# Performance work log

Measured on AMD Instinct MI355X. Metric: run time of the kernel, lower is better.

Reference implementation:

```python
import jax, jax.numpy as jnp
import numpy as np

B, T, D = 2, 2048, 1024
H = 16
HD = D // H  # 128
L = 8  # latent prefix length
SCALE = HD ** -0.5


def setup_inputs() -> dict:
    key = jax.random.key(0)
    ks = jax.random.split(key, 12)
    p = lambda k, shape: jax.random.normal(k, shape, dtype=jnp.float32) * 0.02
    return {
        "hidden_states": jax.random.normal(ks[0], (B, T, D), dtype=jnp.float32),
        "decoder_latent": jax.random.normal(ks[1], (B, H, L, 2 * HD), dtype=jnp.float32),
        "attention_mask": jnp.zeros((B, 1, T, L + T), dtype=jnp.float32),
        "Wq": p(ks[2], (D, D)), "bq": p(ks[3], (D,)),
        "Wk": p(ks[4], (D, D)), "bk": p(ks[5], (D,)),
        "Wv": p(ks[6], (D, D)), "bv": p(ks[7], (D,)),
        "Wo": p(ks[8], (D, D)), "bo": p(ks[9], (D,)),
    }


def _heads(x):
    # [B, S, D] -> [B, H, S, HD]
    return x.reshape(x.shape[0], x.shape[1], H, HD).transpose(0, 2, 1, 3)


def reference(hidden_states, decoder_latent, attention_mask,
              Wq, bq, Wk, bk, Wv, bv, Wo, bo):
    q = _heads((hidden_states @ Wq + bq) * SCALE)            # [B,H,T,HD]
    k = _heads(hidden_states @ Wk + bk)                      # [B,H,T,HD]
    v = _heads(hidden_states @ Wv + bv)
    lk, lv = jnp.split(decoder_latent, 2, axis=-1)           # [B,H,L,HD] each
    k = jnp.concatenate([lk, k], axis=2)                     # [B,H,L+T,HD]
    v = jnp.concatenate([lv, v], axis=2)
    scores = jnp.einsum('bhtd,bhsd->bhts', q, k) + attention_mask
    probs = jax.nn.softmax(scores, axis=-1)                  # [B,H,T,L+T]
    o = jnp.einsum('bhts,bhsd->bhtd', probs, v)              # [B,H,T,HD]
    o = o.transpose(0, 2, 1, 3).reshape(hidden_states.shape[0], -1, D)
    return o @ Wo + bo
```

## Files before the change

### kernel.cpp

```cpp
#include <hip/hip_runtime.h>

#define T_ 2048
#define D_ 1024
#define H_ 16
#define HD_ 64
#define L_ 8
#define S_ 2056
#define M_ 4096
#define SCALE_ 0.125f

typedef unsigned short u16;
typedef u16 u16x4 __attribute__((ext_vector_type(4)));
typedef u16 u16x8 __attribute__((ext_vector_type(8)));
typedef __bf16 bf16x8 __attribute__((ext_vector_type(8)));
typedef float f32x4 __attribute__((ext_vector_type(4)));

#define MFMA(a, b, c) __builtin_amdgcn_mfma_f32_16x16x32_bf16((a), (b), (c), 0, 0, 0)

__device__ __forceinline__ u16 f2bf(float x) {
    unsigned u = __float_as_uint(x);
    return (u16)((u + 0x7fffu + ((u >> 16) & 1u)) >> 16);
}
__device__ __forceinline__ bf16x8 ldfrag(const u16* p) {
    u16x8 u = *(const u16x8*)p;
    return __builtin_bit_cast(bf16x8, u);
}

__global__ __launch_bounds__(256) void cvt_hidden(const float* __restrict__ hs,
                                                  u16* __restrict__ Hh) {
    size_t i4 = (size_t)blockIdx.x * 256 + threadIdx.x;
    f32x4 v = ((const f32x4*)hs)[i4];
    u16x4 hi;
#pragma unroll
    for (int j = 0; j < 4; ++j) hi[j] = f2bf(v[j]);
    ((u16x4*)Hh)[i4] = hi;
}

__global__ __launch_bounds__(256) void tr_w(const float* __restrict__ Wq, const float* __restrict__ Wk,
                                            const float* __restrict__ Wv, const float* __restrict__ Wo,
                                            u16* __restrict__ WT) {
    const int z = blockIdx.z;
    const float* W = (z == 0) ? Wq : (z == 1) ? Wk : (z == 2) ? Wv : Wo;
    u16* WTh = WT + (size_t)z * 1048576u;
    __shared__ float t_s[64][68];
    const int k0 = blockIdx.y * 64, n0 = blockIdx.x * 64;
    const int tid = threadIdx.x;
#pragma unroll
    for (int p = 0; p < 4; ++p) {
        int slot = tid + p * 256;
        int kr = slot >> 4, seg = slot & 15;
        *(f32x4*)&t_s[kr][seg * 4] = *(const f32x4*)(W + (size_t)(k0 + kr) * D_ + n0 + seg * 4);
    }
    __syncthreads();
#pragma unroll
    for (int p = 0; p < 4; ++p) {
        int slot = tid + p * 256;
        int nr = slot >> 4, ks = slot & 15;
        u16x4 hi;
#pragma unroll
        for (int j = 0; j < 4; ++j) hi[j] = f2bf(t_s[ks * 4 + j][nr]);
        *(u16x4*)(WTh + (size_t)(n0 + nr) * D_ + k0 + ks * 4) = hi;
    }
}

__device__ __forceinline__ void gemm_core_1t(const u16* __restrict__ Ah, const u16* __restrict__ BTh,
                                             int bm, int bn, f32x4 acc[4][4]) {
    __shared__ u16 As1[128][40];
    __shared__ u16 Bs1[128][40];
    const int tid = threadIdx.x;
    const int lane = tid & 63, w = tid >> 6;
    const int wm = w >> 1, wn = w & 1;
    const int c = lane & 15, rg = lane >> 4;
    for (int k0 = 0; k0 < D_; k0 += 32) {
        __syncthreads();
#pragma unroll
        for (int i = 0; i < 2; ++i) {
            int slot = tid + i * 256;
            int r = slot >> 2, q = slot & 3;
            *(u16x8*)&As1[r][q * 8] = *(const u16x8*)(Ah + (size_t)(bm * 128 + r) * D_ + k0 + q * 8);
            *(u16x8*)&Bs1[r][q * 8] = *(const u16x8*)(BTh + (size_t)(bn * 128 + r) * D_ + k0 + q * 8);
        }
        __syncthreads();
        bf16x8 af[4], bf[4];
#pragma unroll
        for (int mi = 0; mi < 4; ++mi) af[mi] = ldfrag(&As1[wm * 64 + mi * 16 + c][8 * rg]);
#pragma unroll
        for (int ni = 0; ni < 4; ++ni) bf[ni] = ldfrag(&Bs1[wn * 64 + ni * 16 + c][8 * rg]);
#pragma unroll
        for (int mi = 0; mi < 4; ++mi) {
#pragma unroll
            for (int ni = 0; ni < 4; ++ni) acc[mi][ni] = MFMA(af[mi], bf[ni], acc[mi][ni]);
        }
    }
}

__global__ __launch_bounds__(256) void gemm_qkv(
    const u16* __restrict__ Ah, const u16* __restrict__ WT,
    const float* __restrict__ bq, const float* __restrict__ bk, const float* __restrict__ bv,
    u16* __restrict__ Qh, u16* __restrict__ Kh, u16* __restrict__ Vh) {
    const int z = blockIdx.z;
    const u16* BTh = WT + (size_t)z * 1048576u;
    f32x4 acc[4][4];
    f32x4 zero = {0.f, 0.f, 0.f, 0.f};
#pragma unroll
    for (int a = 0; a < 4; ++a)
#pragma unroll
        for (int b2 = 0; b2 < 4; ++b2) acc[a][b2] = zero;
    gemm_core_1t(Ah, BTh, blockIdx.y, blockIdx.x, acc);
    const int lane = threadIdx.x & 63, w = threadIdx.x >> 6;
    const int wm = w >> 1, wn = w & 1, c = lane & 15, rg = lane >> 4;
    const float* bias = (z == 0) ? bq : ((z == 1) ? bk : bv);
#pragma unroll
    for (int ni = 0; ni < 4; ++ni) {
        int n = blockIdx.x * 128 + wn * 64 + ni * 16 + c;
        float bb = bias[n];
        int hh = n >> 6, hd = n & 63;
#pragma unroll
        for (int mi = 0; mi < 4; ++mi) {
#pragma unroll
            for (int r = 0; r < 4; ++r) {
                int m = blockIdx.y * 128 + wm * 64 + mi * 16 + rg * 4 + r;
                int batch = m >> 11, t = m & 2047;
                float val = acc[mi][ni][r] + bb;
                if (z == 0) {
                    Qh[((size_t)(batch * H_ + hh) * T_ + t) * HD_ + hd] = f2bf(val * SCALE_);
                } else {
                    size_t o = ((size_t)(batch * H_ + hh) * S_ + (t + L_)) * HD_ + hd;
                    if (z == 1) Kh[o] = f2bf(val);
                    else        Vh[o] = f2bf(val);
                }
            }
        }
    }
}

__global__ __launch_bounds__(256) void latent_fill(const float* __restrict__ lat,
                                                   u16* __restrict__ Kh, u16* __restrict__ Vh) {
    int i = blockIdx.x * 256 + threadIdx.x;
    float v = lat[i];
    int cc = i & 127, l = (i >> 7) & 7, h = (i >> 10) & 15, b = i >> 14;
    size_t o = ((size_t)(b * H_ + h) * S_ + l) * HD_ + (cc & 63);
    if (cc < 64) Kh[o] = f2bf(v);
    else         Vh[o] = f2bf(v);
}

__global__ __launch_bounds__(256) void tr_v(const u16* __restrict__ Vh, u16* __restrict__ VTh) {
    const int bh = blockIdx.y;
    const int s0 = blockIdx.x * 64;
    const int tid = threadIdx.x;
    __shared__ u16 t_s[64][72];
#pragma unroll
    for (int p = 0; p < 2; ++p) {
        int slot = tid + p * 256;
        int sr = slot >> 3, seg = slot & 7;
        int s = s0 + sr;
        u16x8 v = {0, 0, 0, 0, 0, 0, 0, 0};
        if (s < S_) v = *(const u16x8*)(Vh + ((size_t)bh * S_ + s) * HD_ + seg * 8);
        *(u16x8*)&t_s[sr][seg * 8] = v;
    }
    __syncthreads();
#pragma unroll
    for (int p = 0; p < 2; ++p) {
        int slot = tid + p * 256;
        int hd = slot & 63, sc = slot >> 6;
        if (s0 + sc * 8 < S_) {
            u16x8 v;
#pragma unroll
            for (int j = 0; j < 8; ++j) v[j] = t_s[sc * 8 + j][hd];
            *(u16x8*)(VTh + ((size_t)bh * HD_ + hd) * S_ + s0 + sc * 8) = v;
        }
    }
}

__global__ __launch_bounds__(256) void attn(
    const u16* __restrict__ Qh, const u16* __restrict__ Kh,
    const u16* __restrict__ VTh, const float* __restrict__ mask, u16* __restrict__ Oh) {
    __shared__ u16 Ks[64][64];
    __shared__ u16 Vs[64][64];
    __shared__ u16 Ps[4][16][64];
    const int tid = threadIdx.x, lane = tid & 63, w = tid >> 6;
    const int bh = blockIdx.y, b = bh >> 4, h = bh & 15;
    const int t0 = blockIdx.x * 64;
    const int c = lane & 15, rg = lane >> 4;
    const int c7 = c & 7;

    bf16x8 qh[2];
    {
        const int t = t0 + w * 16 + c;
        const size_t qbase = ((size_t)bh * T_ + t) * HD_;
        qh[0] = ldfrag(Qh + qbase + 8 * rg);
        qh[1] = ldfrag(Qh + qbase + 32 + 8 * rg);
    }
    f32x4 oa[4];
    f32x4 zero = {0.f, 0.f, 0.f, 0.f};
#pragma unroll
    for (int f = 0; f < 4; ++f) oa[f] = zero;
    float lrun[4] = {0.f, 0.f, 0.f, 0.f};
    const float* mrow[4];
#pragma unroll
    for (int r = 0; r < 4; ++r)
        mrow[r] = mask + ((size_t)b * T_ + t0 + w * 16 + rg * 4 + r) * S_;

    for (int s0 = 0; s0 < S_; s0 += 64) {
        __syncthreads();
#pragma unroll
        for (int i = 0; i < 2; ++i) {
            int slot = tid + i * 256;
            int row = (slot >> 3) & 63, seg = slot & 7;
            int s = s0 + row;
            u16x8 v = {0, 0, 0, 0, 0, 0, 0, 0};
            if (s < S_) v = *(const u16x8*)(Kh + ((size_t)bh * S_ + s) * HD_ + seg * 8);
            *(u16x8*)&Ks[row][(seg ^ (row & 7)) * 8] = v;
        }
#pragma unroll
        for (int i = 0; i < 2; ++i) {
            int slot = tid + i * 256;
            int row = (slot >> 3) & 63, seg = slot & 7;
            int ss = s0 + seg * 8;
            u16x8 v = {0, 0, 0, 0, 0, 0, 0, 0};
            if (ss < S_) v = *(const u16x8*)(VTh + ((size_t)bh * HD_ + row) * S_ + ss);
            *(u16x8*)&Vs[row][(seg ^ (row & 7)) * 8] = v;
        }
        float mreg[4][4];
#pragma unroll
        for (int r = 0; r < 4; ++r) {
#pragma unroll
            for (int cf = 0; cf < 4; ++cf) {
                int sa = s0 + cf * 16 + c;
                mreg[r][cf] = (sa < S_) ? (mrow[r][sa] - 8.0f) : -1e30f;
            }
        }
        __syncthreads();

        f32x4 sc[4];
#pragma unroll
        for (int cf = 0; cf < 4; ++cf) sc[cf] = zero;
#pragma unroll
        for (int ks = 0; ks < 2; ++ks) {
#pragma unroll
            for (int cf = 0; cf < 4; ++cf) {
                int g = ((ks * 4 + rg) ^ c7) * 8;
                bf16x8 kf = ldfrag(&Ks[cf * 16 + c][g]);
                sc[cf] = MFMA(qh[ks], kf, sc[cf]);
            }
        }
#pragma unroll
        for (int r = 0; r < 4; ++r) {
#pragma unroll
            for (int cf = 0; cf < 4; ++cf) sc[cf][r] = __expf(sc[cf][r] + mreg[r][cf]);
            lrun[r] += (sc[0][r] + sc[1][r]) + (sc[2][r] + sc[3][r]);
        }
#pragma unroll
        for (int r = 0; r < 4; ++r) {
            int prow = rg * 4 + r;
#pragma unroll
            for (int cf = 0; cf < 4; ++cf) {
                int pg = (cf * 2 + (c >> 3)) ^ (prow & 7);
                Ps[w][prow][pg * 8 + c7] = (u16)(__float_as_uint(sc[cf][r]) >> 16);
            }
        }
#pragma unroll
        for (int kf = 0; kf < 2; ++kf) {
            int g = ((kf * 4 + rg) ^ c7) * 8;
            bf16x8 pa = ldfrag(&Ps[w][c][g]);
#pragma unroll
            for (int f = 0; f < 4; ++f) {
                bf16x8 vh = ldfrag(&Vs[f * 16 + c][g]);
                oa[f] = MFMA(pa, vh, oa[f]);
            }
        }
    }
#pragma unroll
    for (int mm = 1; mm < 16; mm <<= 1) {
#pragma unroll
        for (int r = 0; r < 4; ++r) lrun[r] += __shfl_xor(lrun[r], mm);
    }
#pragma unroll
    for (int r = 0; r < 4; ++r) lrun[r] = 1.0f / lrun[r];
#pragma unroll
    for (int f = 0; f < 4; ++f) {
#pragma unroll
        for (int r = 0; r < 4; ++r) {
            int tg = t0 + w * 16 + rg * 4 + r;
            int col = h * HD_ + f * 16 + c;
            Oh[((size_t)b * T_ + tg) * D_ + col] = f2bf(oa[f][r] * lrun[r]);
        }
    }
}

__global__ __launch_bounds__(256) void gemm_fin(
    const u16* __restrict__ Ah, const u16* __restrict__ BTh,
    const float* __restrict__ bo, float* __restrict__ out) {
    f32x4 acc[4][4];
    f32x4 zero = {0.f, 0.f, 0.f, 0.f};
#pragma unroll
    for (int a = 0; a < 4; ++a)
#pragma unroll
        for (int b2 = 0; b2 < 4; ++b2) acc[a][b2] = zero;
    gemm_core_1t(Ah, BTh, blockIdx.y, blockIdx.x, acc);
    const int lane = threadIdx.x & 63, w = threadIdx.x >> 6;
    const int wm = w >> 1, wn = w & 1, c = lane & 15, rg = lane >> 4;
#pragma unroll
    for (int ni = 0; ni < 4; ++ni) {
        int n = blockIdx.x * 128 + wn * 64 + ni * 16 + c;
        float bb = bo[n];
#pragma unroll
        for (int mi = 0; mi < 4; ++mi) {
#pragma unroll
            for (int r = 0; r < 4; ++r) {
                int m = blockIdx.y * 128 + wm * 64 + mi * 16 + rg * 4 + r;
                out[(size_t)m * D_ + n] = acc[mi][ni][r] + bb;
            }
        }
    }
}

extern "C" void kernel_launch(void* const* d_in, const int* in_sizes, int n_in,
                              void* d_out, int out_size, void* d_ws, size_t ws_size,
                              hipStream_t stream) {
    (void)in_sizes; (void)n_in; (void)out_size;
    if (ws_size < 50429952ull) return;
    const float* hs  = (const float*)d_in[0];
    const float* lat = (const float*)d_in[1];
    const float* msk = (const float*)d_in[2];
    const float* Wq = (const float*)d_in[3];
    const float* bq = (const float*)d_in[4];
    const float* Wk = (const float*)d_in[5];
    const float* bk = (const float*)d_in[6];
    const float* Wv = (const float*)d_in[7];
    const float* bv = (const float*)d_in[8];
    const float* Wo = (const float*)d_in[9];
    const float* bo = (const float*)d_in[10];
    float* out = (float*)d_out;
    char* ws = (char*)d_ws;

    u16* Hh  = (u16*)(ws + 0ull);
    u16* WT  = (u16*)(ws + 8388608ull);
    u16* Qh  = (u16*)(ws + 16777216ull);
    u16* Kh  = (u16*)(ws + 25165824ull);
    u16* Vh  = (u16*)(ws + 33587200ull);
    u16* VTh = (u16*)(ws + 42008576ull);
    u16* Oh  = Hh;

    cvt_hidden<<<4096, 256, 0, stream>>>(hs, Hh);
    tr_w<<<dim3(16, 16, 4), 256, 0, stream>>>(Wq, Wk, Wv, Wo, WT);
    gemm_qkv<<<dim3(8, 32, 3), 256, 0, stream>>>(Hh, WT, bq, bk, bv, Qh, Kh, Vh);
    latent_fill<<<128, 256, 0, stream>>>(lat, Kh, Vh);
    tr_v<<<dim3(33, 32), 256, 0, stream>>>(Vh, VTh);
    attn<<<dim3(32, 32), 256, 0, stream>>>(Qh, Kh, VTh, msk, Oh);
    gemm_fin<<<dim3(8, 32), 256, 0, stream>>>(Oh, WT + 3u * 1048576u, bo, out);
}
```

Measured before the change: 408.2 us.

## Double-buffer attention K/V tiles with direct global-to-LDS loads

The attention kernel now keeps two LDS buffers for K and V and issues the next tile's loads with global_load_lds (direct to LDS) before computing on the current tile. This drops to one barrier per iteration and lets memory latency overlap with the MFMA and softmax work. Out-of-range rows are clamped to valid addresses instead of zero-filled, which relies on the mask and zero probabilities to cancel them. LDS use doubles for K/V, which may lower occupancy. Correctness also depends on the load-count waits being placed before the barrier.

Result: slower. 464.8 us (+13.9%).

```diff
diff --git a/kernel.cpp b/kernel.cpp
--- a/kernel.cpp
+++ b/kernel.cpp
@@ -24,6 +24,11 @@
 __device__ __forceinline__ bf16x8 ldfrag(const u16* p) {
     u16x8 u = *(const u16x8*)p;
     return __builtin_bit_cast(bf16x8, u);
+}
+__device__ __forceinline__ void g2lds16(const u16* g, u16* l) {
+    __builtin_amdgcn_global_load_lds(
+        (const __attribute__((address_space(1))) void*)g,
+        (__attribute__((address_space(3))) void*)l, 16, 0, 0);
 }
 
 __global__ __launch_bounds__(256) void cvt_hidden(const float* __restrict__ hs,
@@ -175,8 +180,8 @@
 __global__ __launch_bounds__(256) void attn(
     const u16* __restrict__ Qh, const u16* __restrict__ Kh,
     const u16* __restrict__ VTh, const float* __restrict__ mask, u16* __restrict__ Oh) {
-    __shared__ u16 Ks[64][64];
-    __shared__ u16 Vs[64][64];
+    __shared__ u16 Ks[2][64][64];
+    __shared__ u16 Vs[2][64][64];
     __shared__ u16 Ps[4][16][64];
     const int tid = threadIdx.x, lane = tid & 63, w = tid >> 6;
     const int bh = blockIdx.y, b = bh >> 4, h = bh & 15;
@@ -184,6 +189,23 @@
     const int c = lane & 15, rg = lane >> 4;
     const int c7 = c & 7;
 
+    const int srow_o = lane >> 3;
+    const int sseg   = lane & 7;
+
+    auto STAGE = [&](int bufi, int s0n) {
+#pragma unroll
+        for (int i = 0; i < 2; ++i) {
+            int row = w * 16 + i * 8 + srow_o;
+            int sg = sseg ^ (row & 7);
+            int sK = s0n + row;
+            sK = (sK < S_) ? sK : (S_ - 1);
+            g2lds16(Kh + ((size_t)bh * S_ + sK) * HD_ + sg * 8, &Ks[bufi][w * 16 + i * 8][0]);
+            int sV = s0n + sg * 8;
+            sV = (sV <= S_ - 8) ? sV : (S_ - 8);
+            g2lds16(VTh + ((size_t)bh * HD_ + row) * S_ + sV, &Vs[bufi][w * 16 + i * 8][0]);
+        }
+    };
+
     bf16x8 qh[2];
     {
         const int t = t0 + w * 16 + c;
@@ -201,26 +223,14 @@
     for (int r = 0; r < 4; ++r)
         mrow[r] = mask + ((size_t)b * T_ + t0 + w * 16 + rg * 4 + r) * S_;
 
-    for (int s0 = 0; s0 < S_; s0 += 64) {
-        __syncthreads();
-#pragma unroll
-        for (int i = 0; i < 2; ++i) {
-            int slot = tid + i * 256;
-            int row = (slot >> 3) & 63, seg = slot & 7;
-            int s = s0 + row;
-            u16x8 v = {0, 0, 0, 0, 0, 0, 0, 0};
-            if (s < S_) v = *(const u16x8*)(Kh + ((size_t)bh * S_ + s) * HD_ + seg * 8);
-            *(u16x8*)&Ks[row][(seg ^ (row & 7)) * 8] = v;
-        }
-#pragma unroll
-        for (int i = 0; i < 2; ++i) {
-            int slot = tid + i * 256;
-            int row = (slot >> 3) & 63, seg = slot & 7;
-            int ss = s0 + seg * 8;
-            u16x8 v = {0, 0, 0, 0, 0, 0, 0, 0};
-            if (ss < S_) v = *(const u16x8*)(VTh + ((size_t)bh * HD_ + row) * S_ + ss);
-            *(u16x8*)&Vs[row][(seg ^ (row & 7)) * 8] = v;
-        }
+    STAGE(0, 0);
+    __syncthreads();
+    int buf = 0;
+
+    for (int t = 0; t < 33; ++t) {
+        const int s0 = t * 64;
+        if (t + 1 < 33) STAGE(buf ^ 1, s0 + 64);
+
         float mreg[4][4];
 #pragma unroll
         for (int r = 0; r < 4; ++r) {
@@ -230,7 +240,6 @@
                 mreg[r][cf] = (sa < S_) ? (mrow[r][sa] - 8.0f) : -1e30f;
             }
         }
-        __syncthreads();
 
         f32x4 sc[4];
 #pragma unroll
@@ -240,7 +249,7 @@
 #pragma unroll
             for (int cf = 0; cf < 4; ++cf) {
                 int g = ((ks * 4 + rg) ^ c7) * 8;
-                bf16x8 kf = ldfrag(&Ks[cf * 16 + c][g]);
+                bf16x8 kf = ldfrag(&Ks[buf][cf * 16 + c][g]);
                 sc[cf] = MFMA(qh[ks], kf, sc[cf]);
             }
         }
@@ -265,10 +274,12 @@
             bf16x8 pa = ldfrag(&Ps[w][c][g]);
 #pragma unroll
             for (int f = 0; f < 4; ++f) {
-                bf16x8 vh = ldfrag(&Vs[f * 16 + c][g]);
+                bf16x8 vh = ldfrag(&Vs[buf][f * 16 + c][g]);
                 oa[f] = MFMA(pa, vh, oa[f]);
             }
         }
+        __syncthreads();
+        buf ^= 1;
     }
 #pragma unroll
     for (int mm = 1; mm < 16; mm <<= 1) {
```
